# Performance work log

Hardware: AMD Instinct MI355X
Metric: run time of the kernel (lower is better)

## Reference

```python
import jax, jax.numpy as jnp
import numpy as np
import math

B, T, C, H, E = 1, 384, 512, 8, 16
D = C // H

def layer_norm(x, w, b, eps=1e-5):
    mu = jnp.mean(x, axis=-1, keepdims=True)
    var = jnp.mean(jnp.square(x - mu), axis=-1, keepdims=True)
    return (x - mu) * jax.lax.rsqrt(var + eps) * w + b

def setup_inputs() -> dict:
    key = jax.random.key(0)
    ks = jax.random.split(key, 12)
    s = 0.02
    return {
        'x': jax.random.normal(ks[0], (B, T, C), jnp.float32),
        'bias_matrix': jax.random.randint(ks[1], (B, T, T), 0, E, jnp.int32),
        'ln1_w': jnp.ones((C,), jnp.float32),
        'ln1_b': jnp.zeros((C,), jnp.float32),
        'w_attn_w': jax.random.normal(ks[2], (3 * C, C), jnp.float32) * s,
        'w_attn_b': jnp.zeros((3 * C,), jnp.float32),
        'w_proj_w': jax.random.normal(ks[3], (C, C), jnp.float32) * s,
        'w_proj_b': jnp.zeros((C,), jnp.float32),
        'attn_bias_emb': jax.random.normal(ks[4], (E, H), jnp.float32) * s,
        'edge_emb': jax.random.normal(ks[5], (E, C), jnp.float32) * s,
        'w_edge_k_w': jax.random.normal(ks[6], (C, C), jnp.float32) * s,
        'w_edge_k_b': jnp.zeros((C,), jnp.float32),
        'w_edge_v_w': jax.random.normal(ks[7], (C, C), jnp.float32) * s,
        'w_edge_v_b': jnp.zeros((C,), jnp.float32),
        'ln2_w': jnp.ones((C,), jnp.float32),
        'ln2_b': jnp.zeros((C,), jnp.float32),
        'c_fc_w': jax.random.normal(ks[8], (4 * C, C), jnp.float32) * s,
        'c_fc_b': jnp.zeros((4 * C,), jnp.float32),
        'c_proj_w': jax.random.normal(ks[9], (C, 4 * C), jnp.float32) * s,
        'c_proj_b': jnp.zeros((C,), jnp.float32),
    }

def reference(x, bias_matrix, ln1_w, ln1_b, w_attn_w, w_attn_b, w_proj_w, w_proj_b,
              attn_bias_emb, edge_emb, w_edge_k_w, w_edge_k_b, w_edge_v_w, w_edge_v_b,
              ln2_w, ln2_b, c_fc_w, c_fc_b, c_proj_w, c_proj_b):
    # --- attention branch ---
    h = layer_norm(x, ln1_w, ln1_b)
    qkv = h @ w_attn_w.T + w_attn_b                      # (B,T,3C)
    q, k, v = jnp.split(qkv, 3, axis=-1)
    q = q.reshape(B, T, H, D).transpose(0, 2, 1, 3)      # (B,H,T,D)
    k = k.reshape(B, T, H, D).transpose(0, 2, 1, 3)
    v = v.reshape(B, T, H, D).transpose(0, 2, 1, 3)
    scale = math.sqrt(D)

    ee = edge_emb[bias_matrix]                           # (B,T,T,C)
    e_k = (ee @ w_edge_k_w.T + w_edge_k_b).reshape(B, T, T, H, D)
    # score[b,h,i,j] = sum_d q[b,h,i,d] * k[b,h,j,d] * e_k[b,i,j,h,d]
    scores = jnp.einsum('bhid,bhjd,bijhd->bhij', q, k, e_k) / scale

    mask = jnp.tril(jnp.ones((T, T), bool))              # causal, diag included
    scores = jnp.where(mask, scores, -jnp.inf)
    ab = attn_bias_emb[bias_matrix].transpose(0, 3, 1, 2)  # (B,H,T,T)
    ab = jnp.where(mask, ab, 0.0)
    attn = jax.nn.softmax(scores + ab, axis=-1)

    e_v = (ee @ w_edge_v_w.T + w_edge_v_b).reshape(B, T, T, H, D)
    # y[b,h,i,d] = sum_j attn[b,h,i,j] * v[b,h,j,d] * e_v[b,i,j,h,d]
    y = jnp.einsum('bhij,bhjd,bijhd->bhid', attn, v, e_v)
    y = y.transpose(0, 2, 1, 3).reshape(B, T, C)
    y = y @ w_proj_w.T + w_proj_b
    x = x + y

    # --- MLP branch ---
    h2 = layer_norm(x, ln2_w, ln2_b)
    h2 = jax.nn.gelu(h2 @ c_fc_w.T + c_fc_b, approximate=False)
    x = x + (h2 @ c_proj_w.T + c_proj_b)
    return x
```

## Files before the change

### kernel.cpp

```cpp
#include <hip/hip_runtime.h>
#include <math.h>

#define TT 384
#define CC 512
#define HH 8
#define EE 16

typedef __bf16 bf16_t;
typedef __bf16 bf16x8 __attribute__((ext_vector_type(8)));
typedef __bf16 bf16x4v __attribute__((ext_vector_type(4)));
typedef float f32x4 __attribute__((ext_vector_type(4)));

__device__ __forceinline__ float wave_reduce_sum(float v) {
#pragma unroll
  for (int off = 32; off >= 1; off >>= 1) v += __shfl_xor(v, off, 64);
  return v;
}

__device__ __forceinline__ void wrow_unit(const float* __restrict__ wr,
                                          const float* __restrict__ g,
                                          const float* __restrict__ bb,
                                          float extra_c, bf16_t* __restrict__ orow,
                                          float* __restrict__ s1p,
                                          float* __restrict__ cp, int lane) {
  const float* p = wr + lane * 8;
  f32x4 w0 = *(const f32x4*)p, w1 = *(const f32x4*)(p + 4);
  f32x4 g0 = *(const f32x4*)(g + lane * 8), g1 = *(const f32x4*)(g + lane * 8 + 4);
  f32x4 b0 = *(const f32x4*)(bb + lane * 8), b1 = *(const f32x4*)(bb + lane * 8 + 4);
  f32x4 p0 = w0 * g0, p1 = w1 * g1;
  bf16x8 o;
  o[0] = (bf16_t)p0.x; o[1] = (bf16_t)p0.y; o[2] = (bf16_t)p0.z; o[3] = (bf16_t)p0.w;
  o[4] = (bf16_t)p1.x; o[5] = (bf16_t)p1.y; o[6] = (bf16_t)p1.z; o[7] = (bf16_t)p1.w;
  *(bf16x8*)(orow + lane * 8) = o;
  float s1 = p0.x + p0.y + p0.z + p0.w + p1.x + p1.y + p1.z + p1.w;
  float c = w0.x * b0.x + w0.y * b0.y + w0.z * b0.z + w0.w * b0.w +
            w1.x * b1.x + w1.y * b1.y + w1.z * b1.z + w1.w * b1.w;
  s1 = wave_reduce_sum(s1);
  c = wave_reduce_sum(c);
  if (lane == 0) { *s1p = s1; *cp = c + extra_c; }
}

struct PrepX {
  const float *eemb, *wekw, *wekb, *wevw, *wevb;
  const float *ln2w, *ln2b, *cfcw, *cfcb;
  const float *wproj, *wcproj;
  float *ektab, *evtab, *s1f, *cf, *x1s1, *x1s2;
  bf16_t *wfc_bf, *wproj_bf, *wcproj_bf;
};

__device__ void prep_unit(int u, const PrepX& X, int tid) {
  int lane = tid & 63, wave = tid >> 6;
  if (u < 256) {
    int wid = u * 4 + wave;
    int gbase = wid * 16;
    int table = gbase >> 13;
    int e = (gbase >> 9) & 15;
    int c0 = gbase & 511;
    const float* er = X.eemb + e * 512 + lane * 8;
    f32x4 ea = *(const f32x4*)er;
    f32x4 eb = *(const f32x4*)(er + 4);
    const float* wbase = table ? X.wevw : X.wekw;
    const float* bbase = table ? X.wevb : X.wekb;
    float* obase = (table ? X.evtab : X.ektab) + e * 512;
#pragma unroll
    for (int o = 0; o < 16; o++) {
      int c = c0 + o;
      const float* wr = wbase + (size_t)c * 512 + lane * 8;
      f32x4 wa = *(const f32x4*)wr;
      f32x4 wb = *(const f32x4*)(wr + 4);
      float acc = ea.x * wa.x + ea.y * wa.y + ea.z * wa.z + ea.w * wa.w +
                  eb.x * wb.x + eb.y * wb.y + eb.z * wb.z + eb.w * wb.w;
      acc = wave_reduce_sum(acc);
      if (lane == 0) obase[c] = acc + bbase[c];
    }
  } else if (u < 768) {
    int n = (u - 256) * 4 + wave;
    wrow_unit(X.cfcw + (size_t)n * 512, X.ln2w, X.ln2b, X.cfcb[n],
              X.wfc_bf + (size_t)n * 512, X.s1f + n, X.cf + n, lane);
  } else if (u < 1024) {
    int base = (u - 768) * 1024;
    for (int t = tid; t < 1024; t += 256) {
      f32x4 a = *((const f32x4*)X.wcproj + base + t);
      bf16x4v o;
      o[0] = (bf16_t)a.x; o[1] = (bf16_t)a.y; o[2] = (bf16_t)a.z; o[3] = (bf16_t)a.w;
      *((bf16x4v*)X.wcproj_bf + base + t) = o;
    }
  } else if (u < 1088) {
    int base = (u - 1024) * 1024;
    for (int t = tid; t < 1024; t += 256) {
      f32x4 a = *((const f32x4*)X.wproj + base + t);
      bf16x4v o;
      o[0] = (bf16_t)a.x; o[1] = (bf16_t)a.y; o[2] = (bf16_t)a.z; o[3] = (bf16_t)a.w;
      *((bf16x4v*)X.wproj_bf + base + t) = o;
    }
  } else if (u == 1088) {
    for (int i = tid; i < 384; i += 256) { X.x1s1[i] = 0.f; X.x1s2[i] = 0.f; }
  }
}

__global__ __launch_bounds__(256) void qkv_k(
    const float* __restrict__ x, const float* __restrict__ wattn,
    const float* __restrict__ ln1w, const float* __restrict__ ln1b,
    const float* __restrict__ wattnb, bf16_t* __restrict__ out, PrepX X) {
  int tid = threadIdx.x;
  if (blockIdx.y >= 12) {
    prep_unit((blockIdx.y - 12) * gridDim.x + blockIdx.x, X, tid);
    return;
  }
  __shared__ float part[4][32][32];
  __shared__ float rst[2][4][32];
  __shared__ float wst[2][4][32];
  int lane = tid & 63, wave = tid >> 6;
  int m0 = blockIdx.y * 32, n0 = blockIdx.x * 32;
  int r16 = lane & 15, quad = lane >> 4;
  int k0 = wave * 128;

  f32x4 acc[2][2];
  f32x4 zero = {0.f, 0.f, 0.f, 0.f};
#pragma unroll
  for (int i = 0; i < 2; i++)
#pragma unroll
    for (int j = 0; j < 2; j++) acc[i][j] = zero;

  const float* Af = x + (size_t)(m0 + r16) * 512 + k0 + quad * 8;
  const float* Wf = wattn + (size_t)(n0 + r16) * 512 + k0 + quad * 8;
  const float* gp = ln1w + k0 + quad * 8;
  const float* bp = ln1b + k0 + quad * 8;

  float sx[2] = {0.f, 0.f}, sxx[2] = {0.f, 0.f};
  float s1[2] = {0.f, 0.f}, cc[2] = {0.f, 0.f};

  for (int kb0 = 0; kb0 < 128; kb0 += 64) {
    uint4 araw[2][2][2], wraw[2][2][2];
#pragma unroll
    for (int u = 0; u < 2; u++) {
      int kb = kb0 + u * 32;
#pragma unroll
      for (int t = 0; t < 2; t++) {
        araw[u][t][0] = *(const uint4*)(Af + (size_t)t * 16 * 512 + kb);
        araw[u][t][1] = *(const uint4*)(Af + (size_t)t * 16 * 512 + kb + 4);
        wraw[u][t][0] = *(const uint4*)(Wf + (size_t)t * 16 * 512 + kb);
        wraw[u][t][1] = *(const uint4*)(Wf + (size_t)t * 16 * 512 + kb + 4);
      }
    }
#pragma unroll
    for (int u = 0; u < 2; u++) {
      int kb = kb0 + u * 32;
      f32x4 g0 = *(const f32x4*)(gp + kb), g1 = *(const f32x4*)(gp + kb + 4);
      f32x4 b0 = *(const f32x4*)(bp + kb), b1 = *(const f32x4*)(bp + kb + 4);
      bf16x8 af[2], bfr[2];
#pragma unroll
      for (int t = 0; t < 2; t++) {
        f32x4 a0 = *reinterpret_cast<const f32x4*>(&araw[u][t][0]);
        f32x4 a1 = *reinterpret_cast<const f32x4*>(&araw[u][t][1]);
        af[t][0] = (bf16_t)a0.x; af[t][1] = (bf16_t)a0.y;
        af[t][2] = (bf16_t)a0.z; af[t][3] = (bf16_t)a0.w;
        af[t][4] = (bf16_t)a1.x; af[t][5] = (bf16_t)a1.y;
        af[t][6] = (bf16_t)a1.z; af[t][7] = (bf16_t)a1.w;
        sx[t] += a0.x + a0.y + a0.z + a0.w + a1.x + a1.y + a1.z + a1.w;
        sxx[t] += a0.x * a0.x + a0.y * a0.y + a0.z * a0.z + a0.w * a0.w +
                  a1.x * a1.x + a1.y * a1.y + a1.z * a1.z + a1.w * a1.w;
        f32x4 w0 = *reinterpret_cast<const f32x4*>(&wraw[u][t][0]);
        f32x4 w1 = *reinterpret_cast<const f32x4*>(&wraw[u][t][1]);
        f32x4 p0 = w0 * g0, p1 = w1 * g1;
        bfr[t][0] = (bf16_t)p0.x; bfr[t][1] = (bf16_t)p0.y;
        bfr[t][2] = (bf16_t)p0.z; bfr[t][3] = (bf16_t)p0.w;
        bfr[t][4] = (bf16_t)p1.x; bfr[t][5] = (bf16_t)p1.y;
        bfr[t][6] = (bf16_t)p1.z; bfr[t][7] = (bf16_t)p1.w;
        s1[t] += p0.x + p0.y + p0.z + p0.w + p1.x + p1.y + p1.z + p1.w;
        cc[t] += w0.x * b0.x + w0.y * b0.y + w0.z * b0.z + w0.w * b0.w +
                 w1.x * b1.x + w1.y * b1.y + w1.z * b1.z + w1.w * b1.w;
      }
#pragma unroll
      for (int i = 0; i < 2; i++)
#pragma unroll
        for (int j = 0; j < 2; j++)
          acc[i][j] = __builtin_amdgcn_mfma_f32_16x16x32_bf16(af[i], bfr[j],
                                                              acc[i][j], 0, 0, 0);
    }
  }

#pragma unroll
  for (int t = 0; t < 2; t++) {
    sx[t] += __shfl_xor(sx[t], 16, 64);  sx[t] += __shfl_xor(sx[t], 32, 64);
    sxx[t] += __shfl_xor(sxx[t], 16, 64); sxx[t] += __shfl_xor(sxx[t], 32, 64);
    s1[t] += __shfl_xor(s1[t], 16, 64);  s1[t] += __shfl_xor(s1[t], 32, 64);
    cc[t] += __shfl_xor(cc[t], 16, 64);  cc[t] += __shfl_xor(cc[t], 32, 64);
  }
  if (quad == 0) {
#pragma unroll
    for (int t = 0; t < 2; t++) {
      rst[0][wave][t * 16 + r16] = sx[t];
      rst[1][wave][t * 16 + r16] = sxx[t];
      wst[0][wave][t * 16 + r16] = s1[t];
      wst[1][wave][t * 16 + r16] = cc[t];
    }
  }
#pragma unroll
  for (int i = 0; i < 2; i++)
#pragma unroll
    for (int j = 0; j < 2; j++)
#pragma unroll
      for (int r = 0; r < 4; r++)
        part[wave][i * 16 + quad * 4 + r][j * 16 + r16] = acc[i][j][r];
  __syncthreads();

  int row = tid >> 3, c4 = (tid & 7) * 4;
  f32x4 v = *(const f32x4*)&part[0][row][c4];
  v += *(const f32x4*)&part[1][row][c4];
  v += *(const f32x4*)&part[2][row][c4];
  v += *(const f32x4*)&part[3][row][c4];
  float sxt = rst[0][0][row] + rst[0][1][row] + rst[0][2][row] + rst[0][3][row];
  float sxxt = rst[1][0][row] + rst[1][1][row] + rst[1][2][row] + rst[1][3][row];
  float mu = sxt * (1.0f / 512.0f);
  float var = sxxt * (1.0f / 512.0f) - mu * mu;
  float rs = rsqrtf(var + 1e-5f);
  int grow = m0 + row, gcol = n0 + c4;
  bf16x4v o;
#pragma unroll
  for (int t = 0; t < 4; t++) {
    int cl = c4 + t;
    float s1v = wst[0][0][cl] + wst[0][1][cl] + wst[0][2][cl] + wst[0][3][cl];
    float ccv = wst[1][0][cl] + wst[1][1][cl] + wst[1][2][cl] + wst[1][3][cl] +
                wattnb[n0 + cl];
    o[t] = (bf16_t)(rs * (v[t] - mu * s1v) + ccv);
  }
  *(bf16x4v*)(out + (size_t)grow * 1536 + gcol) = o;
}

template <int MODE>
__global__ __launch_bounds__(256) void gemm_k(
    const void* __restrict__ Aptr, const bf16_t* __restrict__ Wb,
    const float* __restrict__ e0, const float* __restrict__ e1,
    const float* __restrict__ e2, const float* __restrict__ e3,
    const float* __restrict__ res, void* __restrict__ out,
    float* __restrict__ st1, float* __restrict__ st2, int N, int K) {
  constexpr bool AF32 = (MODE == 2);
  constexpr int AW = AF32 ? 2 : 1;
  __shared__ float part[4][32][32];
  int tid = threadIdx.x;
  int lane = tid & 63, wave = tid >> 6;
  int m0 = blockIdx.y * 32, n0 = blockIdx.x * 32;
  int r16 = lane & 15, quad = lane >> 4;
  int kchunk = K >> 2, k0 = wave * kchunk;

  f32x4 acc[2][2];
  f32x4 zero = {0.f, 0.f, 0.f, 0.f};
#pragma unroll
  for (int i = 0; i < 2; i++)
#pragma unroll
    for (int j = 0; j < 2; j++) acc[i][j] = zero;

  const float* Af = (const float*)Aptr + (size_t)(m0 + r16) * K + k0 + quad * 8;
  const bf16_t* Ab = (const bf16_t*)Aptr + (size_t)(m0 + r16) * K + k0 + quad * 8;
  const bf16_t* Wp = Wb + (size_t)(n0 + r16) * K + k0 + quad * 8;

  for (int kb0 = 0; kb0 < kchunk; kb0 += 128) {
    uint4 araw[4][2][AW];
    uint4 braw[4][2];
#pragma unroll
    for (int u = 0; u < 4; u++) {
      int kb = kb0 + u * 32;
#pragma unroll
      for (int t = 0; t < 2; t++) {
        if (AF32) {
          araw[u][t][0] = *(const uint4*)(Af + (size_t)t * 16 * K + kb);
          araw[u][t][1] = *(const uint4*)(Af + (size_t)t * 16 * K + kb + 4);
        } else {
          araw[u][t][0] = *(const uint4*)(Ab + (size_t)t * 16 * K + kb);
        }
        braw[u][t] = *(const uint4*)(Wp + (size_t)t * 16 * K + kb);
      }
    }
#pragma unroll
    for (int u = 0; u < 4; u++) {
      bf16x8 af[2], bfr[2];
#pragma unroll
      for (int t = 0; t < 2; t++) {
        if (AF32) {
          f32x4 a = *reinterpret_cast<const f32x4*>(&araw[u][t][0]);
          f32x4 c = *reinterpret_cast<const f32x4*>(&araw[u][t][1]);
          af[t][0] = (bf16_t)a.x; af[t][1] = (bf16_t)a.y;
          af[t][2] = (bf16_t)a.z; af[t][3] = (bf16_t)a.w;
          af[t][4] = (bf16_t)c.x; af[t][5] = (bf16_t)c.y;
          af[t][6] = (bf16_t)c.z; af[t][7] = (bf16_t)c.w;
        } else {
          af[t] = *reinterpret_cast<const bf16x8*>(&araw[u][t][0]);
        }
        bfr[t] = *reinterpret_cast<const bf16x8*>(&braw[u][t]);
      }
#pragma unroll
      for (int i = 0; i < 2; i++)
#pragma unroll
        for (int j = 0; j < 2; j++)
          acc[i][j] = __builtin_amdgcn_mfma_f32_16x16x32_bf16(af[i], bfr[j],
                                                              acc[i][j], 0, 0, 0);
    }
  }

#pragma unroll
  for (int i = 0; i < 2; i++)
#pragma unroll
    for (int j = 0; j < 2; j++)
#pragma unroll
      for (int r = 0; r < 4; r++)
        part[wave][i * 16 + quad * 4 + r][j * 16 + r16] = acc[i][j][r];
  __syncthreads();

  int row = tid >> 3, c4 = (tid & 7) * 4;
  f32x4 v = *(const f32x4*)&part[0][row][c4];
  v += *(const f32x4*)&part[1][row][c4];
  v += *(const f32x4*)&part[2][row][c4];
  v += *(const f32x4*)&part[3][row][c4];
  int grow = m0 + row, gcol = n0 + c4;

  if (MODE == 2) {
    float S = e0[grow], Q = e1[grow];
    float mu = S * (1.0f / 512.0f);
    float var = Q * (1.0f / 512.0f) - mu * mu;
    float rs = rsqrtf(var + 1e-5f);
    f32x4 s1v = *(const f32x4*)(e2 + gcol);
    f32x4 ccv = *(const f32x4*)(e3 + gcol);
    bf16x4v o;
#pragma unroll
    for (int t = 0; t < 4; t++) {
      float xg = rs * (v[t] - mu * s1v[t]) + ccv[t];
      xg = 0.5f * xg * (1.0f + erff(xg * 0.70710678118654752f));
      o[t] = (bf16_t)xg;
    }
    *(bf16x4v*)((bf16_t*)out + (size_t)grow * N + gcol) = o;
  } else {
    v += *(const f32x4*)(e2 + gcol);
    v += *(const f32x4*)(res + (size_t)grow * N + gcol);
    *(f32x4*)((float*)out + (size_t)grow * N + gcol) = v;
    if (MODE == 1) {
      float sv = v.x + v.y + v.z + v.w;
      float qv = v.x * v.x + v.y * v.y + v.z * v.z + v.w * v.w;
      sv += __shfl_down(sv, 4, 8); qv += __shfl_down(qv, 4, 8);
      sv += __shfl_down(sv, 2, 8); qv += __shfl_down(qv, 2, 8);
      sv += __shfl_down(sv, 1, 8); qv += __shfl_down(qv, 1, 8);
      if ((tid & 7) == 0) {
        atomicAdd(st1 + grow, sv);
        atomicAdd(st2 + grow, qv);
      }
    }
  }
}

__global__ __launch_bounds__(256) void attn_k(
    const bf16_t* __restrict__ qkv, const int* __restrict__ bias_matrix,
    const float* __restrict__ attn_bias_emb, const float* __restrict__ ek_tab,
    const float* __restrict__ ev_tab, bf16_t* __restrict__ ybuf) {
  __shared__ float s[TT];
  __shared__ int ebuf[TT];
  __shared__ float qe[EE][68];
  __shared__ float evh[EE * 64];
  __shared__ float red[4 * 64];
  __shared__ float absh[EE];
  __shared__ float scr[4];

  int i = blockIdx.x, h = blockIdx.y;
  int tid = threadIdx.x, lane = tid & 63, wave = tid >> 6;
  int n = i + 1;

  for (int j = tid; j < n; j += 256) ebuf[j] = bias_matrix[i * TT + j];
  if (tid < EE) absh[tid] = attn_bias_emb[tid * HH + h];
  for (int idx = tid; idx < EE * 64; idx += 256) {
    int e = idx >> 6, d = idx & 63;
    float qv = (float)qkv[(size_t)i * 1536 + h * 64 + d];
    qe[e][d] = qv * ek_tab[e * 512 + h * 64 + d];
    evh[idx] = ev_tab[e * 512 + h * 64 + d];
  }
  __syncthreads();

  float ls = 0.0f;
  for (int jl = tid; jl < n; jl += 256) {
    int e = ebuf[jl];
    const uint4* kp = (const uint4*)(qkv + (size_t)jl * 1536 + 512 + h * 64);
    uint4 kr[8];
#pragma unroll
    for (int dg = 0; dg < 8; dg++) kr[dg] = kp[dg];
    float acc = 0.f;
#pragma unroll
    for (int dg = 0; dg < 8; dg++) {
      bf16x8 kv = *reinterpret_cast<const bf16x8*>(&kr[dg]);
      f32x4 qa = *(const f32x4*)&qe[e][dg * 8];
      f32x4 qb = *(const f32x4*)&qe[e][dg * 8 + 4];
      acc += (float)kv[0] * qa.x + (float)kv[1] * qa.y + (float)kv[2] * qa.z +
             (float)kv[3] * qa.w + (float)kv[4] * qb.x + (float)kv[5] * qb.y +
             (float)kv[6] * qb.z + (float)kv[7] * qb.w;
    }
    float p = __expf(acc * 0.125f + absh[e]);
    s[jl] = p;
    ls += p;
  }
  ls = wave_reduce_sum(ls);
  if (lane == 0) scr[wave] = ls;
  __syncthreads();
  float inv = 1.0f / (scr[0] + scr[1] + scr[2] + scr[3]);

  float acc = 0.0f;
  int j = wave;
  for (; j + 4 < n; j += 8) {
    int e0 = ebuf[j], e1 = ebuf[j + 4];
    float p0 = s[j], p1 = s[j + 4];
    float v0 = (float)qkv[(size_t)j * 1536 + 1024 + h * 64 + lane];
    float v1 = (float)qkv[(size_t)(j + 4) * 1536 + 1024 + h * 64 + lane];
    acc += p0 * v0 * evh[e0 * 64 + lane] + p1 * v1 * evh[e1 * 64 + lane];
  }
  for (; j < n; j += 4) {
    int e = ebuf[j];
    float vv = (float)qkv[(size_t)j * 1536 + 1024 + h * 64 + lane];
    acc += s[j] * vv * evh[e * 64 + lane];
  }
  red[wave * 64 + lane] = acc;
  __syncthreads();
  if (tid < 64) {
    float y = (red[tid] + red[64 + tid] + red[128 + tid] + red[192 + tid]) * inv;
    ybuf[(size_t)i * CC + h * 64 + tid] = (bf16_t)y;
  }
}

extern "C" void kernel_launch(void* const* d_in, const int* in_sizes, int n_in,
                              void* d_out, int out_size, void* d_ws,
                              size_t ws_size, hipStream_t stream) {
  const float* x = (const float*)d_in[0];
  const int* bias_mat = (const int*)d_in[1];

  char* wp = (char*)d_ws;
  float* ektab = (float*)wp;  wp += 16 * 512 * 4;
  float* evtab = (float*)wp;  wp += 16 * 512 * 4;
  float* x1s1 = (float*)wp;   wp += 384 * 4;
  float* x1s2 = (float*)wp;   wp += 384 * 4;
  float* s1f = (float*)wp;    wp += 2048 * 4;
  float* cf = (float*)wp;     wp += 2048 * 4;
  float* x1 = (float*)wp;     wp += 384 * 512 * 4;
  bf16_t* wfc_bf = (bf16_t*)wp;    wp += 2048 * 512 * 2;
  bf16_t* wproj_bf = (bf16_t*)wp;  wp += 512 * 512 * 2;
  bf16_t* wcproj_bf = (bf16_t*)wp; wp += 512 * 2048 * 2;
  bf16_t* qkv = (bf16_t*)wp;  wp += 384 * 1536 * 2;
  bf16_t* ybuf = (bf16_t*)wp; wp += 384 * 512 * 2;
  bf16_t* gbuf = (bf16_t*)wp; wp += 384 * 2048 * 2;

  PrepX X;
  X.eemb = (const float*)d_in[9];
  X.wekw = (const float*)d_in[10];
  X.wekb = (const float*)d_in[11];
  X.wevw = (const float*)d_in[12];
  X.wevb = (const float*)d_in[13];
  X.ln2w = (const float*)d_in[14];
  X.ln2b = (const float*)d_in[15];
  X.cfcw = (const float*)d_in[16];
  X.cfcb = (const float*)d_in[17];
  X.wproj = (const float*)d_in[6];
  X.wcproj = (const float*)d_in[18];
  X.ektab = ektab; X.evtab = evtab; X.s1f = s1f; X.cf = cf;
  X.x1s1 = x1s1; X.x1s2 = x1s2;
  X.wfc_bf = wfc_bf; X.wproj_bf = wproj_bf; X.wcproj_bf = wcproj_bf;

  qkv_k<<<dim3(48, 35), 256, 0, stream>>>(
      x, (const float*)d_in[4], (const float*)d_in[2], (const float*)d_in[3],
      (const float*)d_in[5], qkv, X);
  attn_k<<<dim3(TT, HH), 256, 0, stream>>>(qkv, bias_mat,
                                           (const float*)d_in[8], ektab, evtab,
                                           ybuf);
  gemm_k<1><<<dim3(16, 12), 256, 0, stream>>>(
      ybuf, wproj_bf, nullptr, nullptr, (const float*)d_in[7], nullptr, x, x1,
      x1s1, x1s2, 512, 512);
  gemm_k<2><<<dim3(64, 12), 256, 0, stream>>>(x1, wfc_bf, x1s1, x1s2, s1f, cf,
                                              nullptr, gbuf, nullptr, nullptr,
                                              2048, 512);
  gemm_k<3><<<dim3(16, 12), 256, 0, stream>>>(
      gbuf, wcproj_bf, nullptr, nullptr, (const float*)d_in[19], nullptr, x1,
      d_out, nullptr, nullptr, 512, 2048);
}
```

Baseline: 174.9 us.

## Bucket attention keys by edge type to factor out e_v multiply

The attention kernel now builds a per-row histogram of edge types in shared memory. It scatters (byte offset, probability) pairs into edge-type buckets so the PV accumulation sums p*v per bucket and multiplies by the e_v entry once per edge type. The V gather is software-pipelined, and row order is reversed so the longest causal rows launch first. This adds shared-memory atomics, two extra syncs and serial prefix work on one thread in exchange for fewer multiplies and LDS reads of evh.

```diff
diff --git a/kernel.cpp b/kernel.cpp
--- a/kernel.cpp
+++ b/kernel.cpp
@@ -351,25 +351,43 @@
     const bf16_t* __restrict__ qkv, const int* __restrict__ bias_matrix,
     const float* __restrict__ attn_bias_emb, const float* __restrict__ ek_tab,
     const float* __restrict__ ev_tab, bf16_t* __restrict__ ybuf) {
-  __shared__ float s[TT];
   __shared__ int ebuf[TT];
   __shared__ float qe[EE][68];
   __shared__ float evh[EE * 64];
   __shared__ float red[4 * 64];
   __shared__ float absh[EE];
   __shared__ float scr[4];
-
-  int i = blockIdx.x, h = blockIdx.y;
+  __shared__ int hcnt[EE];
+  __shared__ int hrun[EE];
+  __shared__ int cum[EE + 1];
+  __shared__ uint2 packed[TT];
+
+  int i = (TT - 1) - blockIdx.x, h = blockIdx.y;
   int tid = threadIdx.x, lane = tid & 63, wave = tid >> 6;
   int n = i + 1;
 
-  for (int j = tid; j < n; j += 256) ebuf[j] = bias_matrix[i * TT + j];
+  if (tid < EE) hcnt[tid] = 0;
+  __syncthreads();
+
+  for (int j = tid; j < n; j += 256) {
+    int e = bias_matrix[i * TT + j];
+    ebuf[j] = e;
+    atomicAdd(&hcnt[e], 1);
+  }
   if (tid < EE) absh[tid] = attn_bias_emb[tid * HH + h];
   for (int idx = tid; idx < EE * 64; idx += 256) {
     int e = idx >> 6, d = idx & 63;
     float qv = (float)qkv[(size_t)i * 1536 + h * 64 + d];
     qe[e][d] = qv * ek_tab[e * 512 + h * 64 + d];
     evh[idx] = ev_tab[e * 512 + h * 64 + d];
+  }
+  __syncthreads();
+
+  if (tid == 0) {
+    int a = 0;
+#pragma unroll
+    for (int e = 0; e < EE; e++) { cum[e] = a; hrun[e] = a; a += hcnt[e]; }
+    cum[EE] = a;
   }
   __syncthreads();
 
@@ -391,7 +409,11 @@
              (float)kv[6] * qb.z + (float)kv[7] * qb.w;
     }
     float p = __expf(acc * 0.125f + absh[e]);
-    s[jl] = p;
+    int slot = atomicAdd(&hrun[e], 1);
+    uint2 pk;
+    pk.x = (unsigned)(jl * 3072 + 2048 + (h << 7));
+    pk.y = __float_as_uint(p);
+    packed[slot] = pk;
     ls += p;
   }
   ls = wave_reduce_sum(ls);
@@ -399,19 +421,27 @@
   __syncthreads();
   float inv = 1.0f / (scr[0] + scr[1] + scr[2] + scr[3]);
 
+  const char* qbase = (const char*)qkv + 2 * lane;
   float acc = 0.0f;
-  int j = wave;
-  for (; j + 4 < n; j += 8) {
-    int e0 = ebuf[j], e1 = ebuf[j + 4];
-    float p0 = s[j], p1 = s[j + 4];
-    float v0 = (float)qkv[(size_t)j * 1536 + 1024 + h * 64 + lane];
-    float v1 = (float)qkv[(size_t)(j + 4) * 1536 + 1024 + h * 64 + lane];
-    acc += p0 * v0 * evh[e0 * 64 + lane] + p1 * v1 * evh[e1 * 64 + lane];
-  }
-  for (; j < n; j += 4) {
-    int e = ebuf[j];
-    float vv = (float)qkv[(size_t)j * 1536 + 1024 + h * 64 + lane];
-    acc += s[j] * vv * evh[e * 64 + lane];
+#pragma unroll 1
+  for (int e = 0; e < EE; e++) {
+    int b0 = cum[e] + wave;
+    int b1 = cum[e + 1];
+    float evd = evh[e * 64 + lane];
+    float t = 0.0f;
+    if (b0 < b1) {
+      uint2 pk = packed[b0];
+      float vc = (float)*(const bf16_t*)(qbase + pk.x);
+      for (int idx = b0 + 4; idx < b1; idx += 4) {
+        uint2 nx = packed[idx];
+        float vn = (float)*(const bf16_t*)(qbase + nx.x);
+        t = fmaf(__uint_as_float(pk.y), vc, t);
+        pk = nx;
+        vc = vn;
+      }
+      t = fmaf(__uint_as_float(pk.y), vc, t);
+    }
+    acc = fmaf(evd, t, acc);
   }
   red[wave * 64 + lane] = acc;
   __syncthreads();
```

After: 185.0 us. 1.06x slower.

## Pair causal attention rows per block to balance work and share K/V loads

Applied to the files above, without the earlier changes.

Each attention block now handles query row b together with row T-1-b, so every block does the same amount of causal work and the grid is halved. K rows and V values loaded for the longer row are reused for the shorter row, and the bias index and probability are packed together in shared memory. The PV loop is unrolled by four. This aims to remove triangular load imbalance and cut redundant K/V traffic, but it uses more shared memory and registers per block and leaves fewer blocks in the grid.

```diff
diff --git a/kernel.cpp b/kernel.cpp
--- a/kernel.cpp
+++ b/kernel.cpp
@@ -351,73 +351,132 @@
     const bf16_t* __restrict__ qkv, const int* __restrict__ bias_matrix,
     const float* __restrict__ attn_bias_emb, const float* __restrict__ ek_tab,
     const float* __restrict__ ev_tab, bf16_t* __restrict__ ybuf) {
-  __shared__ float s[TT];
-  __shared__ int ebuf[TT];
-  __shared__ float qe[EE][68];
+  __shared__ uint2 ps1[TT], ps2[TT];
+  __shared__ float qe1[EE][68], qe2[EE][68];
   __shared__ float evh[EE * 64];
-  __shared__ float red[4 * 64];
+  __shared__ float red[2][4 * 64];
   __shared__ float absh[EE];
-  __shared__ float scr[4];
-
-  int i = blockIdx.x, h = blockIdx.y;
+  __shared__ float scr[2][4];
+
+  int b = blockIdx.x, h = blockIdx.y;
+  int i1 = b, i2 = (TT - 1) - b;
+  int n1 = i1 + 1, n2 = i2 + 1;
   int tid = threadIdx.x, lane = tid & 63, wave = tid >> 6;
-  int n = i + 1;
-
-  for (int j = tid; j < n; j += 256) ebuf[j] = bias_matrix[i * TT + j];
+
   if (tid < EE) absh[tid] = attn_bias_emb[tid * HH + h];
   for (int idx = tid; idx < EE * 64; idx += 256) {
     int e = idx >> 6, d = idx & 63;
-    float qv = (float)qkv[(size_t)i * 1536 + h * 64 + d];
-    qe[e][d] = qv * ek_tab[e * 512 + h * 64 + d];
+    float q1 = (float)qkv[(size_t)i1 * 1536 + h * 64 + d];
+    float q2 = (float)qkv[(size_t)i2 * 1536 + h * 64 + d];
+    float ek = ek_tab[e * 512 + h * 64 + d];
+    qe1[e][d] = q1 * ek;
+    qe2[e][d] = q2 * ek;
     evh[idx] = ev_tab[e * 512 + h * 64 + d];
   }
   __syncthreads();
 
-  float ls = 0.0f;
-  for (int jl = tid; jl < n; jl += 256) {
-    int e = ebuf[jl];
+  float ls1 = 0.0f, ls2 = 0.0f;
+  const int* bm1 = bias_matrix + (size_t)i1 * TT;
+  const int* bm2 = bias_matrix + (size_t)i2 * TT;
+  for (int jl = tid; jl < n2; jl += 256) {
+    int e2 = bm2[jl];
     const uint4* kp = (const uint4*)(qkv + (size_t)jl * 1536 + 512 + h * 64);
     uint4 kr[8];
 #pragma unroll
     for (int dg = 0; dg < 8; dg++) kr[dg] = kp[dg];
-    float acc = 0.f;
+    float a2 = 0.f;
 #pragma unroll
     for (int dg = 0; dg < 8; dg++) {
       bf16x8 kv = *reinterpret_cast<const bf16x8*>(&kr[dg]);
-      f32x4 qa = *(const f32x4*)&qe[e][dg * 8];
-      f32x4 qb = *(const f32x4*)&qe[e][dg * 8 + 4];
-      acc += (float)kv[0] * qa.x + (float)kv[1] * qa.y + (float)kv[2] * qa.z +
-             (float)kv[3] * qa.w + (float)kv[4] * qb.x + (float)kv[5] * qb.y +
-             (float)kv[6] * qb.z + (float)kv[7] * qb.w;
-    }
-    float p = __expf(acc * 0.125f + absh[e]);
-    s[jl] = p;
-    ls += p;
-  }
-  ls = wave_reduce_sum(ls);
-  if (lane == 0) scr[wave] = ls;
+      f32x4 qa = *(const f32x4*)&qe2[e2][dg * 8];
+      f32x4 qb = *(const f32x4*)&qe2[e2][dg * 8 + 4];
+      a2 += (float)kv[0] * qa.x + (float)kv[1] * qa.y + (float)kv[2] * qa.z +
+            (float)kv[3] * qa.w + (float)kv[4] * qb.x + (float)kv[5] * qb.y +
+            (float)kv[6] * qb.z + (float)kv[7] * qb.w;
+    }
+    float p2 = __expf(a2 * 0.125f + absh[e2]);
+    uint2 pk2; pk2.x = (unsigned)e2; pk2.y = __float_as_uint(p2);
+    ps2[jl] = pk2;
+    ls2 += p2;
+    if (jl < n1) {
+      int e1 = bm1[jl];
+      float a1 = 0.f;
+#pragma unroll
+      for (int dg = 0; dg < 8; dg++) {
+        bf16x8 kv = *reinterpret_cast<const bf16x8*>(&kr[dg]);
+        f32x4 qa = *(const f32x4*)&qe1[e1][dg * 8];
+        f32x4 qb = *(const f32x4*)&qe1[e1][dg * 8 + 4];
+        a1 += (float)kv[0] * qa.x + (float)kv[1] * qa.y + (float)kv[2] * qa.z +
+              (float)kv[3] * qa.w + (float)kv[4] * qb.x + (float)kv[5] * qb.y +
+              (float)kv[6] * qb.z + (float)kv[7] * qb.w;
+      }
+      float p1 = __expf(a1 * 0.125f + absh[e1]);
+      uint2 pk1; pk1.x = (unsigned)e1; pk1.y = __float_as_uint(p1);
+      ps1[jl] = pk1;
+      ls1 += p1;
+    }
+  }
+  ls1 = wave_reduce_sum(ls1);
+  ls2 = wave_reduce_sum(ls2);
+  if (lane == 0) { scr[0][wave] = ls1; scr[1][wave] = ls2; }
   __syncthreads();
-  float inv = 1.0f / (scr[0] + scr[1] + scr[2] + scr[3]);
-
-  float acc = 0.0f;
+  float inv1 = 1.0f / (scr[0][0] + scr[0][1] + scr[0][2] + scr[0][3]);
+  float inv2 = 1.0f / (scr[1][0] + scr[1][1] + scr[1][2] + scr[1][3]);
+
+  const bf16_t* vb = qkv + 1024 + h * 64 + lane;
+  float acc1 = 0.0f, acc2 = 0.0f;
   int j = wave;
-  for (; j + 4 < n; j += 8) {
-    int e0 = ebuf[j], e1 = ebuf[j + 4];
-    float p0 = s[j], p1 = s[j + 4];
-    float v0 = (float)qkv[(size_t)j * 1536 + 1024 + h * 64 + lane];
-    float v1 = (float)qkv[(size_t)(j + 4) * 1536 + 1024 + h * 64 + lane];
-    acc += p0 * v0 * evh[e0 * 64 + lane] + p1 * v1 * evh[e1 * 64 + lane];
-  }
-  for (; j < n; j += 4) {
-    int e = ebuf[j];
-    float vv = (float)qkv[(size_t)j * 1536 + 1024 + h * 64 + lane];
-    acc += s[j] * vv * evh[e * 64 + lane];
-  }
-  red[wave * 64 + lane] = acc;
+  for (; j + 12 < n1; j += 16) {
+    float v0 = (float)vb[(size_t)j * 1536];
+    float v1 = (float)vb[(size_t)(j + 4) * 1536];
+    float v2 = (float)vb[(size_t)(j + 8) * 1536];
+    float v3 = (float)vb[(size_t)(j + 12) * 1536];
+    uint2 c0 = ps2[j], c1 = ps2[j + 4], c2 = ps2[j + 8], c3 = ps2[j + 12];
+    uint2 d0 = ps1[j], d1 = ps1[j + 4], d2 = ps1[j + 8], d3 = ps1[j + 12];
+    acc2 = fmaf(__uint_as_float(c0.y) * v0, evh[c0.x * 64 + lane], acc2);
+    acc2 = fmaf(__uint_as_float(c1.y) * v1, evh[c1.x * 64 + lane], acc2);
+    acc2 = fmaf(__uint_as_float(c2.y) * v2, evh[c2.x * 64 + lane], acc2);
+    acc2 = fmaf(__uint_as_float(c3.y) * v3, evh[c3.x * 64 + lane], acc2);
+    acc1 = fmaf(__uint_as_float(d0.y) * v0, evh[d0.x * 64 + lane], acc1);
+    acc1 = fmaf(__uint_as_float(d1.y) * v1, evh[d1.x * 64 + lane], acc1);
+    acc1 = fmaf(__uint_as_float(d2.y) * v2, evh[d2.x * 64 + lane], acc1);
+    acc1 = fmaf(__uint_as_float(d3.y) * v3, evh[d3.x * 64 + lane], acc1);
+  }
+  for (; j < n1; j += 4) {
+    float v0 = (float)vb[(size_t)j * 1536];
+    uint2 c0 = ps2[j], d0 = ps1[j];
+    acc2 = fmaf(__uint_as_float(c0.y) * v0, evh[c0.x * 64 + lane], acc2);
+    acc1 = fmaf(__uint_as_float(d0.y) * v0, evh[d0.x * 64 + lane], acc1);
+  }
+  for (; j + 12 < n2; j += 16) {
+    float v0 = (float)vb[(size_t)j * 1536];
+    float v1 = (float)vb[(size_t)(j + 4) * 1536];
+    float v2 = (float)vb[(size_t)(j + 8) * 1536];
+    float v3 = (float)vb[(size_t)(j + 12) * 1536];
+    uint2 c0 = ps2[j], c1 = ps2[j + 4], c2 = ps2[j + 8], c3 = ps2[j + 12];
+    acc2 = fmaf(__uint_as_float(c0.y) * v0, evh[c0.x * 64 + lane], acc2);
+    acc2 = fmaf(__uint_as_float(c1.y) * v1, evh[c1.x * 64 + lane], acc2);
+    acc2 = fmaf(__uint_as_float(c2.y) * v2, evh[c2.x * 64 + lane], acc2);
+    acc2 = fmaf(__uint_as_float(c3.y) * v3, evh[c3.x * 64 + lane], acc2);
+  }
+  for (; j < n2; j += 4) {
+    float v0 = (float)vb[(size_t)j * 1536];
+    uint2 c0 = ps2[j];
+    acc2 = fmaf(__uint_as_float(c0.y) * v0, evh[c0.x * 64 + lane], acc2);
+  }
+  red[0][wave * 64 + lane] = acc1;
+  red[1][wave * 64 + lane] = acc2;
   __syncthreads();
   if (tid < 64) {
-    float y = (red[tid] + red[64 + tid] + red[128 + tid] + red[192 + tid]) * inv;
-    ybuf[(size_t)i * CC + h * 64 + tid] = (bf16_t)y;
+    float y =
+        (red[0][tid] + red[0][64 + tid] + red[0][128 + tid] + red[0][192 + tid]) *
+        inv1;
+    ybuf[(size_t)i1 * CC + h * 64 + tid] = (bf16_t)y;
+  } else if (tid < 128) {
+    int t = tid - 64;
+    float y =
+        (red[1][t] + red[1][64 + t] + red[1][128 + t] + red[1][192 + t]) * inv2;
+    ybuf[(size_t)i2 * CC + h * 64 + t] = (bf16_t)y;
   }
 }
 
@@ -461,9 +520,9 @@
   qkv_k<<<dim3(48, 35), 256, 0, stream>>>(
       x, (const float*)d_in[4], (const float*)d_in[2], (const float*)d_in[3],
       (const float*)d_in[5], qkv, X);
-  attn_k<<<dim3(TT, HH), 256, 0, stream>>>(qkv, bias_mat,
-                                           (const float*)d_in[8], ektab, evtab,
-                                           ybuf);
+  attn_k<<<dim3(TT / 2, HH), 256, 0, stream>>>(qkv, bias_mat,
+                                               (const float*)d_in[8], ektab,
+                                               evtab, ybuf);
   gemm_k<1><<<dim3(16, 12), 256, 0, stream>>>(
       ybuf, wproj_bf, nullptr, nullptr, (const float*)d_in[7], nullptr, x, x1,
       x1s1, x1s2, 512, 512);
```

Measured after the change: 167.3 us, median of 2. 4.4% less time.
